# Optimization experiments

Hardware: AMD Instinct MI355X
Metric: run time of the kernel (lower is better)

The kernel has to match this reference:

```python
import jax, jax.numpy as jnp
import numpy as np

N = 100000
IN_DIM = 1280
HID = 128
EPS = 1e-5

def _gconv(x, src, dst, W, b, n):
    # DGL GraphConv, norm='both': D_out^{-1/2} gather -> sum -> D_in^{-1/2}, then W, b.
    # Project first (in_feats >= out_feats here) so edge messages are HID-dim.
    ones = jnp.ones(src.shape[0], dtype=x.dtype)
    out_deg = jnp.clip(jax.ops.segment_sum(ones, src, num_segments=n), 1.0)
    in_deg = jnp.clip(jax.ops.segment_sum(ones, dst, num_segments=n), 1.0)
    h = (x * (out_deg ** -0.5)[:, None]) @ W          # [n, HID]
    agg = jax.ops.segment_sum(h[src], dst, num_segments=n)  # scatter-add over edges
    return agg * (in_deg ** -0.5)[:, None] + b

def _batchnorm(x, g, b):
    m = x.mean(0)
    v = jnp.mean((x - m) ** 2, axis=0)  # biased variance (torch BN normalization)
    return (x - m) * jax.lax.rsqrt(v + EPS) * g + b

def _layer(x, edges, W, b, fcW, fcb, g, beta, n):
    # HeteroGraphConv aggregate='sum' over 3 relations, then FC + ReLU + BN
    h = _gconv(x, edges[0][0], edges[0][1], W[0], b[0], n)
    h = h + _gconv(x, edges[1][0], edges[1][1], W[1], b[1], n)
    h = h + _gconv(x, edges[2][0], edges[2][1], W[2], b[2], n)
    h = h @ fcW + fcb
    h = jax.nn.relu(h)
    return _batchnorm(h, g, beta)

def setup_inputs() -> dict:
    key = jax.random.key(0)
    ks = jax.random.split(key, 16)
    x = jax.random.normal(ks[0], (N, IN_DIM), dtype=jnp.float32)
    seq_edges = jax.random.randint(ks[1], (2, 200000), 0, N, dtype=jnp.int32)
    knn_edges = jax.random.randint(ks[2], (2, 1000000), 0, N, dtype=jnp.int32)
    dis_edges = jax.random.randint(ks[3], (2, 1600000), 0, N, dtype=jnp.int32)
    s_in = 1.0 / np.sqrt(IN_DIM)
    s_h = 1.0 / np.sqrt(HID)
    W0 = jax.random.normal(ks[4], (3, IN_DIM, HID), dtype=jnp.float32) * s_in
    b0 = jnp.zeros((3, HID), dtype=jnp.float32)
    fcW0 = jax.random.normal(ks[5], (HID, HID), dtype=jnp.float32) * s_h
    fcb0 = jnp.zeros((HID,), dtype=jnp.float32)
    g0 = jnp.ones((HID,), dtype=jnp.float32)
    beta0 = jnp.zeros((HID,), dtype=jnp.float32)
    W1 = jax.random.normal(ks[6], (3, HID, HID), dtype=jnp.float32) * s_h
    b1 = jnp.zeros((3, HID), dtype=jnp.float32)
    fcW1 = jax.random.normal(ks[7], (HID, HID), dtype=jnp.float32) * s_h
    fcb1 = jnp.zeros((HID,), dtype=jnp.float32)
    g1 = jnp.ones((HID,), dtype=jnp.float32)
    beta1 = jnp.zeros((HID,), dtype=jnp.float32)
    return {"x": x, "seq_edges": seq_edges, "knn_edges": knn_edges, "dis_edges": dis_edges,
            "W0": W0, "b0": b0, "fcW0": fcW0, "fcb0": fcb0, "g0": g0, "beta0": beta0,
            "W1": W1, "b1": b1, "fcW1": fcW1, "fcb1": fcb1, "g1": g1, "beta1": beta1}

def reference(x, seq_edges, knn_edges, dis_edges,
              W0, b0, fcW0, fcb0, g0, beta0,
              W1, b1, fcW1, fcb1, g1, beta1):
    edges = [seq_edges, knn_edges, dis_edges]
    n = x.shape[0]
    h = _layer(x, edges, W0, b0, fcW0, fcb0, g0, beta0, n)
    # dropout after non-final layers is identity at eval
    h = _layer(h, edges, W1, b1, fcW1, fcb1, g1, beta1, n)
    return h
```

## Files before the change

kernel.cpp:

```cpp
#include <hip/hip_runtime.h>
#include <hip/hip_bf16.h>
#include <math.h>

#define NN 100000
#define HID 128
#define EPSV 1e-5f

typedef short bf16x8 __attribute__((ext_vector_type(8)));
typedef float f32x4 __attribute__((ext_vector_type(4)));
typedef unsigned short u16;

__device__ __forceinline__ u16 f2b(float f) {
  unsigned u = __builtin_bit_cast(unsigned, f);
  u += 0x7FFFu + ((u >> 16) & 1u);
  return (u16)(u >> 16);
}
__device__ __forceinline__ float b2f(u16 h) {
  unsigned u = ((unsigned)h) << 16;
  return __builtin_bit_cast(float, u);
}

#define AS1(p) ((__attribute__((address_space(1))) void*)(p))
#define AS3(p) ((__attribute__((address_space(3))) void*)(p))


static __global__ void k_zero(float* __restrict__ p, int n) {
  int i = blockIdx.x * blockDim.x + threadIdx.x;
  if (i < n) p[i] = 0.f;
}

static __global__ void k_zero_i(int* __restrict__ p, int n) {
  int i = blockIdx.x * blockDim.x + threadIdx.x;
  if (i < n) p[i] = 0;
}

static __global__ void k_deg(const int* __restrict__ src, const int* __restrict__ dst,
                             int E, float* __restrict__ outdeg, float* __restrict__ indeg) {
  int e = blockIdx.x * blockDim.x + threadIdx.x;
  if (e < E) {
    atomicAdd(&outdeg[src[e]], 1.f);
    atomicAdd(&indeg[dst[e]], 1.f);
  }
}

static __global__ void k_counts(const float* __restrict__ indegRaw, int* __restrict__ counts, int n3) {
  int i = blockIdx.x * blockDim.x + threadIdx.x;
  if (i < n3) counts[i] = (int)indegRaw[i];
  else if (i == n3) counts[i] = 0;
}

static __global__ void k_rsqrt_clip(float* __restrict__ p, int n) {
  int i = blockIdx.x * blockDim.x + threadIdx.x;
  if (i < n) p[i] = rsqrtf(fmaxf(p[i], 1.f));
}

static __global__ void k_scan1(const int* __restrict__ in, int* __restrict__ out,
                               int* __restrict__ aux, int n) {
  __shared__ int s[256];
  int t = threadIdx.x, i = blockIdx.x * 256 + t;
  int v = (i < n) ? in[i] : 0;
  s[t] = v; __syncthreads();
#pragma unroll
  for (int d = 1; d < 256; d <<= 1) {
    int x = (t >= d) ? s[t - d] : 0;
    __syncthreads();
    s[t] += x;
    __syncthreads();
  }
  if (i < n) out[i] = s[t] - v;
  if (t == 255) aux[blockIdx.x] = s[255];
}

static __global__ void k_scan2(int* __restrict__ aux, int nb) {
  __shared__ int s[256];
  __shared__ int carry;
  int t = threadIdx.x;
  if (t == 0) carry = 0;
  __syncthreads();
  for (int base = 0; base < nb; base += 256) {
    int i = base + t;
    int v = (i < nb) ? aux[i] : 0;
    s[t] = v; __syncthreads();
#pragma unroll
    for (int d = 1; d < 256; d <<= 1) {
      int x = (t >= d) ? s[t - d] : 0;
      __syncthreads();
      s[t] += x;
      __syncthreads();
    }
    int excl = s[t] - v + carry;
    if (i < nb) aux[i] = excl;
    int tot = s[255];
    __syncthreads();
    if (t == 0) carry += tot;
    __syncthreads();
  }
}

static __global__ void k_scan3(int* __restrict__ out, const int* __restrict__ aux, int n) {
  int i = blockIdx.x * 256 + threadIdx.x;
  if (i < n) out[i] += aux[blockIdx.x];
}

static __global__ void k_fill(const int* __restrict__ src, const int* __restrict__ dst, int E,
                              const int* __restrict__ off, int* __restrict__ cur,
                              int rbase, int* __restrict__ srt) {
  int e = blockIdx.x * blockDim.x + threadIdx.x;
  if (e < E) {
    int d = dst[e];
    int p = off[rbase + d] + atomicAdd(&cur[rbase + d], 1);
    srt[p] = src[e];
  }
}

static __global__ void k_cvt_w(const float* __restrict__ W, u16* __restrict__ Wt, int K) {
  int i = blockIdx.x * blockDim.x + threadIdx.x;
  int tot = 3 * K * 128;
  if (i < tot) {
    int rel = i / (K * 128);
    int rem = i - rel * K * 128;
    int k = rem >> 7;
    int c = rem & 127;
    Wt[((size_t)rel * 128 + c) * K + k] = f2b(W[i]);
  }
}

static __global__ void k_cvt_fcw(const float* __restrict__ W, u16* __restrict__ Bt) {
  int i = blockIdx.x * blockDim.x + threadIdx.x;
  if (i < 128 * 128) {
    int k = i >> 7, c = i & 127;
    Bt[c * 128 + k] = f2b(W[i]);
  }
}

template<int K, bool AF32>
__global__ __launch_bounds__(256, 3)
void k_gemm2p(const void* __restrict__ Av,
              const u16* __restrict__ Wt,
              const float* __restrict__ sout,
              u16* __restrict__ Y,
              int M, int NT)
{
  constexpr int A_U16 = AF32 ? 8192 : 4096;
  constexpr int B_U16 = 4096;
  __shared__ u16 lds[2][A_U16 + B_U16];

  const int bid  = blockIdx.x;
  const int xcd  = bid & 7;
  const int s    = bid >> 3;
  const int rel  = s % 3;
  const int tile = xcd + 8 * (s / 3);
  if (tile >= NT) return;
  const int row0 = tile * 128;

  const int t    = threadIdx.x;
  const int lane = t & 63;
  const int w    = t >> 6;
  const int wm   = w >> 1, wn = w & 1;
  const int l15  = lane & 15, l4 = lane >> 4;
  const int kl   = l4 * 8;
  const int nk   = K / 32;

  const u16* Wr = Wt + (size_t)rel * 128 * K;

  int r0 = row0 + (2 * w) * 16 + l15;      if (r0 >= M) r0 = M - 1;
  int r1 = row0 + (2 * w + 1) * 16 + l15;  if (r1 >= M) r1 = M - 1;

  const u16* gb0 = Wr + (size_t)((2 * w) * 16 + l15) * K + kl;
  const u16* gb1 = Wr + (size_t)((2 * w + 1) * 16 + l15) * K + kl;

  const float* Af = (const float*)Av;
  const u16*   Ab = (const u16*)Av;

  auto STAGE = [&](int buf, int k0) {
    u16* L = &lds[buf][0];
    if constexpr (AF32) {
      const float* sa0 = Af + (size_t)r0 * K + k0 + kl;
      const float* sa1 = Af + (size_t)r1 * K + k0 + kl;
      __builtin_amdgcn_global_load_lds(AS1(sa0),     AS3(L + (2 * w) * 1024),       16, 0, 0);
      __builtin_amdgcn_global_load_lds(AS1(sa0 + 4), AS3(L + (2 * w) * 1024 + 512), 16, 0, 0);
      __builtin_amdgcn_global_load_lds(AS1(sa1),     AS3(L + (2 * w + 1) * 1024),       16, 0, 0);
      __builtin_amdgcn_global_load_lds(AS1(sa1 + 4), AS3(L + (2 * w + 1) * 1024 + 512), 16, 0, 0);
    } else {
      const u16* sa0 = Ab + (size_t)r0 * K + k0 + kl;
      const u16* sa1 = Ab + (size_t)r1 * K + k0 + kl;
      __builtin_amdgcn_global_load_lds(AS1(sa0), AS3(L + (2 * w) * 512),     16, 0, 0);
      __builtin_amdgcn_global_load_lds(AS1(sa1), AS3(L + (2 * w + 1) * 512), 16, 0, 0);
    }
    u16* Bd = L + A_U16;
    __builtin_amdgcn_global_load_lds(AS1(gb0 + k0), AS3(Bd + (2 * w) * 512),     16, 0, 0);
    __builtin_amdgcn_global_load_lds(AS1(gb1 + k0), AS3(Bd + (2 * w + 1) * 512), 16, 0, 0);
  };

  f32x4 acc[4][4];
#pragma unroll
  for (int m = 0; m < 4; ++m)
#pragma unroll
    for (int n = 0; n < 4; ++n) acc[m][n] = (f32x4){0.f, 0.f, 0.f, 0.f};

  STAGE(0, 0);

  for (int k = 0; k < nk; ++k) {
    asm volatile("s_waitcnt vmcnt(0)" ::: "memory");
    __builtin_amdgcn_sched_barrier(0);
    __builtin_amdgcn_s_barrier();
    __builtin_amdgcn_sched_barrier(0);

    if (k + 1 < nk) STAGE((k + 1) & 1, (k + 1) * 32);

    const int cur = k & 1;
    bf16x8 a[4], b[4];
    if constexpr (AF32) {
      const float* Al = (const float*)&lds[cur][0];
#pragma unroll
      for (int m = 0; m < 4; ++m) {
        f32x4 lo = *(const f32x4*)&Al[(wm * 4 + m) * 512 + lane * 4];
        f32x4 hi = *(const f32x4*)&Al[(wm * 4 + m) * 512 + 256 + lane * 4];
        union { bf16x8 v; u16 u[8]; } q;
#pragma unroll
        for (int j = 0; j < 4; ++j) {
          q.u[j]     = __builtin_bit_cast(u16, __float2bfloat16(lo[j]));
          q.u[4 + j] = __builtin_bit_cast(u16, __float2bfloat16(hi[j]));
        }
        a[m] = q.v;
      }
    } else {
      const u16* Al = &lds[cur][0];
#pragma unroll
      for (int m = 0; m < 4; ++m) a[m] = *(const bf16x8*)&Al[(wm * 4 + m) * 512 + lane * 8];
    }
    {
      const u16* Bl = &lds[cur][A_U16];
#pragma unroll
      for (int n = 0; n < 4; ++n) b[n] = *(const bf16x8*)&Bl[(wn * 4 + n) * 512 + lane * 8];
    }

#pragma unroll
    for (int m = 0; m < 4; ++m)
#pragma unroll
      for (int n = 0; n < 4; ++n)
        acc[m][n] = __builtin_amdgcn_mfma_f32_16x16x32_bf16(a[m], b[n], acc[m][n], 0, 0, 0);
  }

#pragma unroll
  for (int m = 0; m < 4; ++m) {
    const int rb = row0 + wm * 64 + m * 16 + l4 * 4;
#pragma unroll
    for (int j = 0; j < 4; ++j) {
      const int row = rb + j;
      if (row < M) {
        const float sc = sout[(size_t)rel * NN + row];
        u16* yp = Y + (size_t)row * 384 + rel * 128 + wn * 64 + l15;
#pragma unroll
        for (int n = 0; n < 4; ++n) yp[n * 16] = f2b(acc[m][n][j] * sc);
      }
    }
  }
}

static __global__ __launch_bounds__(256)
void k_gather(const int* __restrict__ off, const int* __restrict__ srt,
              const float* __restrict__ sin_, const u16* __restrict__ Y,
              const float* __restrict__ b, u16* __restrict__ acc16)
{
  int d = blockIdx.x * 4 + (threadIdx.x >> 6);
  if (d >= NN) return;
  int c = (threadIdx.x & 63) * 2;
  float v0 = b[c]     + b[128 + c]     + b[256 + c];
  float v1 = b[c + 1] + b[128 + c + 1] + b[256 + c + 1];
#pragma unroll
  for (int r = 0; r < 3; ++r) {
    int base = r * NN + d;
    int j0 = off[base], j1 = off[base + 1];
    float p0 = 0.f, p1 = 0.f;
    int j = j0;
    for (; j + 4 <= j1; j += 4) {
      int s0 = srt[j], s1 = srt[j + 1], s2 = srt[j + 2], s3 = srt[j + 3];
      unsigned u0 = *(const unsigned*)&Y[(size_t)s0 * 384 + r * 128 + c];
      unsigned u1 = *(const unsigned*)&Y[(size_t)s1 * 384 + r * 128 + c];
      unsigned u2 = *(const unsigned*)&Y[(size_t)s2 * 384 + r * 128 + c];
      unsigned u3 = *(const unsigned*)&Y[(size_t)s3 * 384 + r * 128 + c];
      p0 += b2f((u16)(u0 & 0xFFFFu)) + b2f((u16)(u1 & 0xFFFFu))
          + b2f((u16)(u2 & 0xFFFFu)) + b2f((u16)(u3 & 0xFFFFu));
      p1 += b2f((u16)(u0 >> 16)) + b2f((u16)(u1 >> 16))
          + b2f((u16)(u2 >> 16)) + b2f((u16)(u3 >> 16));
    }
    for (; j < j1; ++j) {
      int s = srt[j];
      unsigned u = *(const unsigned*)&Y[(size_t)s * 384 + r * 128 + c];
      p0 += b2f((u16)(u & 0xFFFFu));
      p1 += b2f((u16)(u >> 16));
    }
    float sc = sin_[base];
    v0 += p0 * sc;
    v1 += p1 * sc;
  }
  unsigned out = (unsigned)f2b(v0) | ((unsigned)f2b(v1) << 16);
  *(unsigned*)&acc16[(size_t)d * 128 + c] = out;
}

static __global__ __launch_bounds__(512)
void k_fc_mfma(const u16* __restrict__ A,
               const u16* __restrict__ Bt,
               const float* __restrict__ bias,
               float* __restrict__ Z, int M)
{
  __shared__ u16 Ab[4][4096];

  const int row0 = blockIdx.x * 128;
  const int t    = threadIdx.x;
  const int lane = t & 63;
  const int w    = t >> 6;
  const int wm   = w >> 2;
  const int wn   = w & 3;
  const int l15  = lane & 15, l4 = lane >> 4;
  const int kl   = l4 * 8;

  int ar = row0 + w * 16 + l15;  if (ar >= M) ar = M - 1;

  bf16x8 br[2][4];
#pragma unroll
  for (int n = 0; n < 2; ++n)
#pragma unroll
    for (int ks = 0; ks < 4; ++ks)
      br[n][ks] = *(const bf16x8*)&Bt[(size_t)(wn * 32 + n * 16 + l15) * 128 + ks * 32 + kl];

#pragma unroll
  for (int ks = 0; ks < 4; ++ks)
    __builtin_amdgcn_global_load_lds(AS1(A + (size_t)ar * 128 + ks * 32 + kl),
                                     AS3(&Ab[ks][w * 512]), 16, 0, 0);

  asm volatile("s_waitcnt vmcnt(0)" ::: "memory");
  __syncthreads();

  f32x4 acc[4][2];
#pragma unroll
  for (int m = 0; m < 4; ++m) { acc[m][0] = (f32x4){0,0,0,0}; acc[m][1] = (f32x4){0,0,0,0}; }

#pragma unroll
  for (int ks = 0; ks < 4; ++ks) {
#pragma unroll
    for (int m = 0; m < 4; ++m) {
      bf16x8 a = *(const bf16x8*)&Ab[ks][(wm * 4 + m) * 512 + lane * 8];
      acc[m][0] = __builtin_amdgcn_mfma_f32_16x16x32_bf16(a, br[0][ks], acc[m][0], 0, 0, 0);
      acc[m][1] = __builtin_amdgcn_mfma_f32_16x16x32_bf16(a, br[1][ks], acc[m][1], 0, 0, 0);
    }
  }

#pragma unroll
  for (int m = 0; m < 4; ++m) {
    const int rb = row0 + wm * 64 + m * 16 + l4 * 4;
#pragma unroll
    for (int j = 0; j < 4; ++j) {
      const int row = rb + j;
      if (row < M) {
#pragma unroll
        for (int n = 0; n < 2; ++n) {
          const int cc = wn * 32 + n * 16 + l15;
          Z[(size_t)row * 128 + cc] = fmaxf(acc[m][n][j] + bias[cc], 0.f);
        }
      }
    }
  }
}

static __global__ void k_bn_stats(const float* __restrict__ Z, int M, float* __restrict__ stats) {
  int col = threadIdx.x;
  float s = 0.f, s2 = 0.f;
  for (int row = blockIdx.x; row < M; row += gridDim.x) {
    float v = Z[(size_t)row * 128 + col];
    s += v;
    s2 += v * v;
  }
  atomicAdd(&stats[col], s);
  atomicAdd(&stats[128 + col], s2);
}

static __global__ void k_bn_finalize(const float* __restrict__ stats, int M,
                                     const float* __restrict__ g, const float* __restrict__ beta,
                                     float* __restrict__ ab) {
  int j = threadIdx.x;
  float m  = stats[j] / (float)M;
  float v  = stats[128 + j] / (float)M - m * m;
  float inv = rsqrtf(v + EPSV) * g[j];
  ab[j]       = inv;
  ab[128 + j] = beta[j] - m * inv;
}

template<bool OUT_BF16>
static __global__ void k_bn_apply(const float* __restrict__ Z, const float* __restrict__ ab,
                                  void* __restrict__ out, int n) {
  int i = blockIdx.x * blockDim.x + threadIdx.x;
  if (i < n) {
    int j = i & 127;
    float v = Z[i] * ab[j] + ab[128 + j];
    if constexpr (OUT_BF16) ((u16*)out)[i] = f2b(v);
    else                    ((float*)out)[i] = v;
  }
}


template<int K, bool AF32, bool OUT_BF16>
static void run_layer(const void* X,
                      const u16* Wt, const float* b,
                      const u16* fcWt, const float* fcb,
                      const float* g, const float* beta,
                      const int* off, const int* srt,
                      float* sOut, float* sIn, u16* Y, float* Z, u16* acc16,
                      float* stats, float* ab, void* out, hipStream_t stream)
{
  const int NT = (NN + 127) / 128;
  const int nblk = 24 * ((NT + 7) / 8);
  k_gemm2p<K, AF32><<<nblk, 256, 0, stream>>>(X, Wt, sOut, Y, NN, NT);

  k_gather<<<(NN + 3) / 4, 256, 0, stream>>>(off, srt, sIn, Y, b, acc16);

  k_fc_mfma<<<NT, 512, 0, stream>>>(acc16, fcWt, fcb, Z, NN);

  k_zero<<<1, 256, 0, stream>>>(stats, 256);
  k_bn_stats<<<1024, 128, 0, stream>>>(Z, NN, stats);
  k_bn_finalize<<<1, 128, 0, stream>>>(stats, NN, g, beta, ab);
  k_bn_apply<OUT_BF16><<<(NN * HID + 255) / 256, 256, 0, stream>>>(Z, ab, out, NN * HID);
}

extern "C" void kernel_launch(void* const* d_in, const int* in_sizes, int n_in,
                              void* d_out, int out_size, void* d_ws, size_t ws_size,
                              hipStream_t stream)
{
  const float* x    = (const float*)d_in[0];
  const int*   seq  = (const int*)d_in[1];
  const int*   knn  = (const int*)d_in[2];
  const int*   dis  = (const int*)d_in[3];
  const float* W0   = (const float*)d_in[4];
  const float* b0   = (const float*)d_in[5];
  const float* fcW0 = (const float*)d_in[6];
  const float* fcb0 = (const float*)d_in[7];
  const float* g0   = (const float*)d_in[8];
  const float* be0  = (const float*)d_in[9];
  const float* W1   = (const float*)d_in[10];
  const float* b1   = (const float*)d_in[11];
  const float* fcW1 = (const float*)d_in[12];
  const float* fcb1 = (const float*)d_in[13];
  const float* g1   = (const float*)d_in[14];
  const float* be1  = (const float*)d_in[15];

  const int E[3] = { in_sizes[1] / 2, in_sizes[2] / 2, in_sizes[3] / 2 };
  const int* srcs[3] = { seq, knn, dis };

  const size_t N = NN;
  const int M3 = 3 * NN;

  float* ws    = (float*)d_ws;
  float* sOut  = ws;
  float* sIn   = sOut + 3 * N;
  u16*   acc16 = (u16*)(sIn + 3 * N);
  float* accF  = (float*)acc16;
  float* stats = accF + N * 128;
  float* ab    = stats + 256;
  u16*   Y     = (u16*)(ab + 256);
  float* Z     = (float*)Y;
  u16*   h16   = Y + N * 384;
  u16*   Wt0   = h16 + N * 128;
  u16*   Wt1   = Wt0 + 3 * 128 * 1280;
  u16*   fcWt0 = Wt1 + 3 * 128 * 128;
  u16*   fcWt1 = fcWt0 + 128 * 128;
  int*   counts= (int*)(fcWt1 + 128 * 128);
  int*   off   = counts + (M3 + 1);
  int*   aux   = off + (M3 + 1);
  int*   cur   = aux + 1536;
  int*   srt   = cur + M3;

  k_cvt_w<<<(3 * 1280 * 128 + 255) / 256, 256, 0, stream>>>(W0, Wt0, 1280);
  k_cvt_w<<<(3 * 128 * 128 + 255) / 256, 256, 0, stream>>>(W1, Wt1, 128);
  k_cvt_fcw<<<(128 * 128 + 255) / 256, 256, 0, stream>>>(fcW0, fcWt0);
  k_cvt_fcw<<<(128 * 128 + 255) / 256, 256, 0, stream>>>(fcW1, fcWt1);

  k_zero<<<(6 * NN + 255) / 256, 256, 0, stream>>>(sOut, 6 * NN);
  for (int r = 0; r < 3; ++r) {
    k_deg<<<(E[r] + 255) / 256, 256, 0, stream>>>(
        srcs[r], srcs[r] + E[r], E[r], sOut + (size_t)r * N, sIn + (size_t)r * N);
  }
  k_counts<<<(M3 + 1 + 255) / 256, 256, 0, stream>>>(sIn, counts, M3);
  k_rsqrt_clip<<<(6 * NN + 255) / 256, 256, 0, stream>>>(sOut, 6 * NN);

  const int nsc = M3 + 1;
  const int nb  = (nsc + 255) / 256;
  k_scan1<<<nb, 256, 0, stream>>>(counts, off, aux, nsc);
  k_scan2<<<1, 256, 0, stream>>>(aux, nb);
  k_scan3<<<nb, 256, 0, stream>>>(off, aux, nsc);

  k_zero_i<<<(M3 + 255) / 256, 256, 0, stream>>>(cur, M3);
  for (int r = 0; r < 3; ++r) {
    k_fill<<<(E[r] + 255) / 256, 256, 0, stream>>>(
        srcs[r], srcs[r] + E[r], E[r], off, cur, r * NN, srt);
  }

  run_layer<1280, true, true>(x, Wt0, b0, fcWt0, fcb0, g0, be0, off, srt,
                              sOut, sIn, Y, Z, acc16, stats, ab, h16, stream);

  run_layer<128, false, false>(h16, Wt1, b1, fcWt1, fcb1, g1, be1, off, srt,
                               sOut, sIn, Y, Z, acc16, stats, ab, d_out, stream);
}
```

Baseline: 1.360 ms.

## Merge per-relation CSR into one tagged CSR and triple-buffer GEMM loads

Builds a single CSR over destination nodes for all three relations. Each source index carries a 2-bit relation tag, so the gather kernel walks one edge list per node with an 8-wide unrolled load batch and picks the per-relation in-degree scale per edge. Separately, the projection GEMM moves from double to triple-buffered LDS staging with partial vmcnt waits, prefetching two K-steps ahead. The occupancy hint is dropped to allow the larger LDS footprint. The tag packing assumes source indices fit in 30 bits, and the extra LDS may reduce resident blocks.

Measured after the change: 1.265 ms. 7.0% less time.

```diff
diff --git a/kernel.cpp b/kernel.cpp
--- a/kernel.cpp
+++ b/kernel.cpp
@@ -43,10 +43,10 @@
   }
 }
 
-static __global__ void k_counts(const float* __restrict__ indegRaw, int* __restrict__ counts, int n3) {
-  int i = blockIdx.x * blockDim.x + threadIdx.x;
-  if (i < n3) counts[i] = (int)indegRaw[i];
-  else if (i == n3) counts[i] = 0;
+static __global__ void k_counts_tot(const float* __restrict__ indegRaw, int* __restrict__ counts, int n) {
+  int i = blockIdx.x * blockDim.x + threadIdx.x;
+  if (i < n) counts[i] = (int)(indegRaw[i] + indegRaw[n + i] + indegRaw[2 * n + i]);
+  else if (i == n) counts[i] = 0;
 }
 
 static __global__ void k_rsqrt_clip(float* __restrict__ p, int n) {
@@ -104,12 +104,12 @@
 
 static __global__ void k_fill(const int* __restrict__ src, const int* __restrict__ dst, int E,
                               const int* __restrict__ off, int* __restrict__ cur,
-                              int rbase, int* __restrict__ srt) {
+                              int rel, int* __restrict__ srt) {
   int e = blockIdx.x * blockDim.x + threadIdx.x;
   if (e < E) {
     int d = dst[e];
-    int p = off[rbase + d] + atomicAdd(&cur[rbase + d], 1);
-    srt[p] = src[e];
+    int p = off[d] + atomicAdd(&cur[d], 1);
+    srt[p] = (src[e] << 2) | rel;
   }
 }
 
@@ -134,7 +134,7 @@
 }
 
 template<int K, bool AF32>
-__global__ __launch_bounds__(256, 3)
+__global__ __launch_bounds__(256)
 void k_gemm2p(const void* __restrict__ Av,
               const u16* __restrict__ Wt,
               const float* __restrict__ sout,
@@ -143,13 +143,13 @@
 {
   constexpr int A_U16 = AF32 ? 8192 : 4096;
   constexpr int B_U16 = 4096;
-  __shared__ u16 lds[2][A_U16 + B_U16];
+  __shared__ u16 lds[3][A_U16 + B_U16];
 
   const int bid  = blockIdx.x;
   const int xcd  = bid & 7;
-  const int s    = bid >> 3;
-  const int rel  = s % 3;
-  const int tile = xcd + 8 * (s / 3);
+  const int sidx = bid >> 3;
+  const int rel  = sidx % 3;
+  const int tile = xcd + 8 * (sidx / 3);
   if (tile >= NT) return;
   const int row0 = tile * 128;
 
@@ -199,16 +199,22 @@
     for (int n = 0; n < 4; ++n) acc[m][n] = (f32x4){0.f, 0.f, 0.f, 0.f};
 
   STAGE(0, 0);
+  if (nk > 1) STAGE(1, 32);
 
   for (int k = 0; k < nk; ++k) {
-    asm volatile("s_waitcnt vmcnt(0)" ::: "memory");
+    if (k + 1 < nk) {
+      if constexpr (AF32) asm volatile("s_waitcnt vmcnt(6)" ::: "memory");
+      else                asm volatile("s_waitcnt vmcnt(4)" ::: "memory");
+    } else {
+      asm volatile("s_waitcnt vmcnt(0)" ::: "memory");
+    }
     __builtin_amdgcn_sched_barrier(0);
     __builtin_amdgcn_s_barrier();
     __builtin_amdgcn_sched_barrier(0);
 
-    if (k + 1 < nk) STAGE((k + 1) & 1, (k + 1) * 32);
-
-    const int cur = k & 1;
+    if (k + 2 < nk) STAGE((k + 2) % 3, (k + 2) * 32);
+
+    const int cur = k % 3;
     bf16x8 a[4], b[4];
     if constexpr (AF32) {
       const float* Al = (const float*)&lds[cur][0];
@@ -268,35 +274,35 @@
   int c = (threadIdx.x & 63) * 2;
   float v0 = b[c]     + b[128 + c]     + b[256 + c];
   float v1 = b[c + 1] + b[128 + c + 1] + b[256 + c + 1];
-#pragma unroll
-  for (int r = 0; r < 3; ++r) {
-    int base = r * NN + d;
-    int j0 = off[base], j1 = off[base + 1];
-    float p0 = 0.f, p1 = 0.f;
-    int j = j0;
-    for (; j + 4 <= j1; j += 4) {
-      int s0 = srt[j], s1 = srt[j + 1], s2 = srt[j + 2], s3 = srt[j + 3];
-      unsigned u0 = *(const unsigned*)&Y[(size_t)s0 * 384 + r * 128 + c];
-      unsigned u1 = *(const unsigned*)&Y[(size_t)s1 * 384 + r * 128 + c];
-      unsigned u2 = *(const unsigned*)&Y[(size_t)s2 * 384 + r * 128 + c];
-      unsigned u3 = *(const unsigned*)&Y[(size_t)s3 * 384 + r * 128 + c];
-      p0 += b2f((u16)(u0 & 0xFFFFu)) + b2f((u16)(u1 & 0xFFFFu))
-          + b2f((u16)(u2 & 0xFFFFu)) + b2f((u16)(u3 & 0xFFFFu));
-      p1 += b2f((u16)(u0 >> 16)) + b2f((u16)(u1 >> 16))
-          + b2f((u16)(u2 >> 16)) + b2f((u16)(u3 >> 16));
-    }
-    for (; j < j1; ++j) {
-      int s = srt[j];
-      unsigned u = *(const unsigned*)&Y[(size_t)s * 384 + r * 128 + c];
-      p0 += b2f((u16)(u & 0xFFFFu));
-      p1 += b2f((u16)(u >> 16));
-    }
-    float sc = sin_[base];
-    v0 += p0 * sc;
-    v1 += p1 * sc;
-  }
-  unsigned out = (unsigned)f2b(v0) | ((unsigned)f2b(v1) << 16);
-  *(unsigned*)&acc16[(size_t)d * 128 + c] = out;
+  const float sc0 = sin_[d], sc1 = sin_[NN + d], sc2 = sin_[2 * NN + d];
+  int j0 = off[d], j1 = off[d + 1];
+  int j = j0;
+  for (; j + 8 <= j1; j += 8) {
+    unsigned uu[8];
+    int rr[8];
+#pragma unroll
+    for (int q = 0; q < 8; ++q) {
+      int tg = srt[j + q];
+      rr[q] = tg & 3;
+      uu[q] = *(const unsigned*)&Y[(size_t)(tg >> 2) * 384 + (size_t)rr[q] * 128 + c];
+    }
+#pragma unroll
+    for (int q = 0; q < 8; ++q) {
+      float s = (rr[q] == 0) ? sc0 : ((rr[q] == 1) ? sc1 : sc2);
+      v0 = fmaf(b2f((u16)(uu[q] & 0xFFFFu)), s, v0);
+      v1 = fmaf(b2f((u16)(uu[q] >> 16)), s, v1);
+    }
+  }
+  for (; j < j1; ++j) {
+    int tg = srt[j];
+    int r = tg & 3;
+    unsigned u = *(const unsigned*)&Y[(size_t)(tg >> 2) * 384 + (size_t)r * 128 + c];
+    float s = (r == 0) ? sc0 : ((r == 1) ? sc1 : sc2);
+    v0 = fmaf(b2f((u16)(u & 0xFFFFu)), s, v0);
+    v1 = fmaf(b2f((u16)(u >> 16)), s, v1);
+  }
+  unsigned o = (unsigned)f2b(v0) | ((unsigned)f2b(v1) << 16);
+  *(unsigned*)&acc16[(size_t)d * 128 + c] = o;
 }
 
 static __global__ __launch_bounds__(512)
@@ -448,7 +454,6 @@
   const int* srcs[3] = { seq, knn, dis };
 
   const size_t N = NN;
-  const int M3 = 3 * NN;
 
   float* ws    = (float*)d_ws;
   float* sOut  = ws;
@@ -465,10 +470,10 @@
   u16*   fcWt0 = Wt1 + 3 * 128 * 128;
   u16*   fcWt1 = fcWt0 + 128 * 128;
   int*   counts= (int*)(fcWt1 + 128 * 128);
-  int*   off   = counts + (M3 + 1);
-  int*   aux   = off + (M3 + 1);
+  int*   off   = counts + (NN + 1);
+  int*   aux   = off + (NN + 1);
   int*   cur   = aux + 1536;
-  int*   srt   = cur + M3;
+  int*   srt   = cur + NN;
 
   k_cvt_w<<<(3 * 1280 * 128 + 255) / 256, 256, 0, stream>>>(W0, Wt0, 1280);
   k_cvt_w<<<(3 * 128 * 128 + 255) / 256, 256, 0, stream>>>(W1, Wt1, 128);
@@ -480,19 +485,19 @@
     k_deg<<<(E[r] + 255) / 256, 256, 0, stream>>>(
         srcs[r], srcs[r] + E[r], E[r], sOut + (size_t)r * N, sIn + (size_t)r * N);
   }
-  k_counts<<<(M3 + 1 + 255) / 256, 256, 0, stream>>>(sIn, counts, M3);
+  k_counts_tot<<<(NN + 1 + 255) / 256, 256, 0, stream>>>(sIn, counts, NN);
   k_rsqrt_clip<<<(6 * NN + 255) / 256, 256, 0, stream>>>(sOut, 6 * NN);
 
-  const int nsc = M3 + 1;
+  const int nsc = NN + 1;
   const int nb  = (nsc + 255) / 256;
   k_scan1<<<nb, 256, 0, stream>>>(counts, off, aux, nsc);
   k_scan2<<<1, 256, 0, stream>>>(aux, nb);
   k_scan3<<<nb, 256, 0, stream>>>(off, aux, nsc);
 
-  k_zero_i<<<(M3 + 255) / 256, 256, 0, stream>>>(cur, M3);
+  k_zero_i<<<(NN + 255) / 256, 256, 0, stream>>>(cur, NN);
   for (int r = 0; r < 3; ++r) {
     k_fill<<<(E[r] + 255) / 256, 256, 0, stream>>>(
-        srcs[r], srcs[r] + E[r], E[r], off, cur, r * NN, srt);
+        srcs[r], srcs[r] + E[r], E[r], off, cur, r, srt);
   }
 
   run_layer<1280, true, true>(x, Wt0, b0, fcWt0, fcb0, g0, be0, off, srt,
```
